# Performance work log

Hardware: AMD Instinct MI355X
Metric: run time of the kernel (lower is better)

The kernel has to match this reference:

```python
import jax, jax.numpy as jnp
import numpy as np

TOP_K = 48
NUM_RBF = 16
MAX_REL = 32  # max_relative_feature
B, L = 2, 3072

# atom order in stacked tensor: N=0, Ca=1, C=2, O=3, Cb=4
_PAIRS = np.array([
    (0, 0), (2, 2), (3, 3), (4, 4), (1, 0), (1, 2), (1, 3), (1, 4),
    (0, 2), (0, 3), (0, 4), (4, 2), (4, 3), (3, 2), (0, 1), (2, 1),
    (3, 1), (4, 1), (2, 0), (3, 0), (4, 0), (2, 4), (3, 4), (2, 3)], dtype=np.int32)


def _rbf(D):
    # D [..., ] -> [..., NUM_RBF]
    mu = jnp.linspace(2.0, 22.0, NUM_RBF)
    sigma = (22.0 - 2.0) / NUM_RBF
    return jnp.exp(-(((D[..., None] - mu) / sigma) ** 2))


def setup_inputs() -> dict:
    key = jax.random.key(0)
    ks = jax.random.split(key, 8)
    X = jax.random.normal(ks[0], (B, L, 4, 3), dtype=jnp.float32) * 3.0
    mask = jnp.ones((B, L), dtype=jnp.float32)
    R_idx = jnp.sort(jax.random.randint(ks[1], (B, L), 0, 6144), axis=-1)
    chain_labels = jax.random.randint(ks[2], (B, L), 0, 4)
    pos_W = jax.random.normal(ks[3], (2 * MAX_REL + 2, 16), dtype=jnp.float32) * 0.1
    pos_b = jax.random.normal(ks[4], (16,), dtype=jnp.float32) * 0.02
    edge_W = jax.random.normal(ks[5], (16 + 25 * NUM_RBF, 128), dtype=jnp.float32) * 0.05
    ln_gamma = jnp.ones((128,), dtype=jnp.float32)
    ln_beta = jnp.zeros((128,), dtype=jnp.float32)
    return {"X": X, "mask": mask, "R_idx": R_idx, "chain_labels": chain_labels,
            "pos_W": pos_W, "pos_b": pos_b, "edge_W": edge_W,
            "ln_gamma": ln_gamma, "ln_beta": ln_beta}


def reference(X, mask, R_idx, chain_labels, pos_W, pos_b, edge_W, ln_gamma, ln_beta):
    # virtual Cb construction
    bvec = X[:, :, 1, :] - X[:, :, 0, :]
    cvec = X[:, :, 2, :] - X[:, :, 1, :]
    avec = jnp.cross(bvec, cvec)
    Ca = X[:, :, 1, :]
    Cb = -0.58273431 * avec + 0.56802827 * bvec - 0.54067466 * cvec + Ca
    atoms = jnp.stack([X[:, :, 0, :], Ca, X[:, :, 2, :], X[:, :, 3, :], Cb], axis=2)  # [B,L,5,3]

    # masked pairwise Ca distances + k smallest neighbors
    mask2d = mask[:, :, None] * mask[:, None, :]                        # [B,L,L]
    dX = Ca[:, :, None, :] - Ca[:, None, :, :]
    D = mask2d * jnp.sqrt(jnp.sum(dX ** 2, axis=-1) + 1e-6)
    D_max = jnp.max(D, axis=-1, keepdims=True)
    D_adjust = D + (1.0 - mask2d) * D_max
    k = min(TOP_K, X.shape[1])
    neg_vals, E_idx = jax.lax.top_k(-D_adjust, k)                       # [B,L,K]
    D_neighbors = -neg_vals

    # gather neighbor atom coords once: [B,L,K,5,3]
    atoms_nb = jax.vmap(lambda a, i: a[i])(atoms, E_idx)

    # 24 remaining atom-pair distances, restricted to neighbors (same math as
    # full cdist + gather since dist is computed per (i, E_idx[i,j]) pair)
    ai, bi = _PAIRS[:, 0], _PAIRS[:, 1]
    diff = atoms[:, :, None, ai, :] - atoms_nb[:, :, :, bi, :]          # [B,L,K,24,3]
    D24 = jnp.sqrt(jnp.sum(diff ** 2, axis=-1) + 1e-6)                  # [B,L,K,24]

    D_all = jnp.concatenate([D_neighbors[..., None], D24], axis=-1)    # [B,L,K,25]
    RBF_all = _rbf(D_all).reshape(D_all.shape[:3] + (25 * NUM_RBF,))   # [B,L,K,400]

    # positional encodings on neighbor offsets
    offset = R_idx[:, :, None] - R_idx[:, None, :]
    offset = jnp.take_along_axis(offset, E_idx, axis=2)                 # [B,L,K]
    same_chain = (chain_labels[:, :, None] - chain_labels[:, None, :] == 0).astype(jnp.int32)
    E_chains = jnp.take_along_axis(same_chain, E_idx, axis=2)           # [B,L,K]
    d = jnp.clip(offset + MAX_REL, 0, 2 * MAX_REL) * E_chains + (1 - E_chains) * (2 * MAX_REL + 1)
    E_positional = pos_W[d] + pos_b                                     # one-hot @ W == row gather

    E = jnp.concatenate([E_positional, RBF_all], axis=-1)              # [B,L,K,416]
    E = E @ edge_W                                                      # [B,L,K,128]
    mu = jnp.mean(E, axis=-1, keepdims=True)
    var = jnp.mean((E - mu) ** 2, axis=-1, keepdims=True)
    E = (E - mu) / jnp.sqrt(var + 1e-5) * ln_gamma + ln_beta
    return E, E_idx
```

## Files before the change

### kernel.cpp

```cpp
#include <hip/hip_runtime.h>
#include <hip/hip_bf16.h>
#include <stdint.h>
#include <math.h>

#define B_   2
#define L_   3072
#define K_   48
#define FDIM 416
#define NOUT 128
#define FRS8 424

__device__ const unsigned char PAIRC[24] = {
    0, 18, 27, 36, 8, 10, 11, 12, 2, 3, 4, 34, 35, 26,
    1, 17, 25, 33, 16, 24, 32, 20, 28, 19
};

typedef __attribute__((ext_vector_type(4))) float f32x4;

__global__ __launch_bounds__(256) void k_prep(const float* __restrict__ X,
                                              const float* __restrict__ edgeW,
                                              float* __restrict__ atoms,
                                              float* __restrict__ CaA,
                                              unsigned char* __restrict__ Wt8)
{
    const int bid = blockIdx.x;
    if (bid < 52) {
        int idx4 = bid * 256 + threadIdx.x;
        int b = idx4 * 4;
        int e0  = b & 7;
        int lhi = (b >> 3) & 3;
        int l15 = (b >> 5) & 15;
        int nt  = (b >> 9) & 7;
        int kt  = b >> 12;
        int n = nt * 16 + l15;
        int kbase = kt * 32 + lhi * 8 + e0;
        float v0 = edgeW[(kbase + 0) * NOUT + n];
        float v1 = edgeW[(kbase + 1) * NOUT + n];
        float v2 = edgeW[(kbase + 2) * NOUT + n];
        float v3 = edgeW[(kbase + 3) * NOUT + n];
        int w = __builtin_amdgcn_cvt_pk_fp8_f32(v0, v1, 0, false);
        w = __builtin_amdgcn_cvt_pk_fp8_f32(v2, v3, w, true);
        ((unsigned int*)Wt8)[idx4] = (unsigned int)w;
    } else {
        int row = (bid - 52) * 256 + threadIdx.x;
        if (row >= B_ * L_) return;
        const float* x = X + row * 12;
        float nx = x[0], ny = x[1], nz = x[2];
        float cax = x[3], cay = x[4], caz = x[5];
        float cx = x[6], cy = x[7], cz = x[8];
        float ox = x[9], oy = x[10], oz = x[11];
        float bx = cax - nx, by = cay - ny, bz = caz - nz;
        float vx = cx - cax, vy = cy - cay, vz = cz - caz;
        float axv = by * vz - bz * vy;
        float ayv = bz * vx - bx * vz;
        float azv = bx * vy - by * vx;
        float cbx = -0.58273431f * axv + 0.56802827f * bx - 0.54067466f * vx + cax;
        float cby = -0.58273431f * ayv + 0.56802827f * by - 0.54067466f * vy + cay;
        float cbz = -0.58273431f * azv + 0.56802827f * bz - 0.54067466f * vz + caz;
        float* A = atoms + row * 16;
        A[0] = nx;  A[1] = ny;  A[2] = nz;
        A[3] = cax; A[4] = cay; A[5] = caz;
        A[6] = cx;  A[7] = cy;  A[8] = cz;
        A[9] = ox;  A[10] = oy; A[11] = oz;
        A[12] = cbx; A[13] = cby; A[14] = cbz;
        A[15] = 0.f;
        CaA[row * 3 + 0] = cax;
        CaA[row * 3 + 1] = cay;
        CaA[row * 3 + 2] = caz;
    }
}

__global__ __launch_bounds__(256) void k_topk(const float* __restrict__ CaA,
                                              const float* __restrict__ mask,
                                              int* __restrict__ eidx,
                                              float* __restrict__ dnb,
                                              float* __restrict__ out_eidx_f)
{
    __shared__ __align__(16) unsigned int SH[3072];
    unsigned int* hist  = SH;
    unsigned int* candJ = SH + 2048;
    unsigned long long* candK = (unsigned long long*)SH;
    __shared__ unsigned int swave[4];
    __shared__ int sP;
    __shared__ unsigned int sCnt;

    const int row = blockIdx.x;
    const int b = row / L_;
    const int tid = threadIdx.x;
    const int lane = tid & 63;
    const int wv = tid >> 6;

    #pragma unroll
    for (int i = 0; i < 8; ++i) hist[tid + 256 * i] = 0;
    if (tid == 0) sCnt = 0;

    const float caxf = CaA[row * 3 + 0];
    const float cayf = CaA[row * 3 + 1];
    const float cazf = CaA[row * 3 + 2];
    const float mif = mask[row];
    const float* Cb = CaA + (size_t)b * L_ * 3;
    const float* mb = mask + (size_t)b * L_;
    __syncthreads();

    unsigned int bits[12];
    #pragma unroll
    for (int m = 0; m < 12; ++m) {
        int j = tid + 256 * m;
        float dx = caxf - Cb[j * 3 + 0];
        float dy = cayf - Cb[j * 3 + 1];
        float dz = cazf - Cb[j * 3 + 2];
        float s = fmaf(dz, dz, fmaf(dy, dy, dx * dx)) + 1e-6f;
        float dist = sqrtf(s);
        bool live = (mif * mb[j]) != 0.0f;
        bits[m] = live ? __float_as_uint(dist) : 0x7F800000u;
        atomicAdd(&hist[bits[m] >> 20], 1u);
    }
    __syncthreads();

    unsigned int loc[8];
    unsigned int s = 0;
    #pragma unroll
    for (int i = 0; i < 8; ++i) { loc[i] = hist[tid * 8 + i]; s += loc[i]; }
    unsigned int sc = s;
    #pragma unroll
    for (int off = 1; off < 64; off <<= 1) {
        unsigned int o = __shfl_up(sc, off);
        if (lane >= off) sc += o;
    }
    if (lane == 63) swave[wv] = sc;
    __syncthreads();
    unsigned int base = 0;
    #pragma unroll
    for (int w = 0; w < 4; ++w) if (w < wv) base += swave[w];
    unsigned int cum = base + sc - s;
    #pragma unroll
    for (int i = 0; i < 8; ++i) {
        unsigned int c = loc[i];
        if (cum < K_ && cum + c >= K_) sP = tid * 8 + i;
        cum += c;
    }
    __syncthreads();
    const unsigned int Pth = (unsigned int)sP + 2;

    #pragma unroll
    for (int m = 0; m < 12; ++m) {
        if ((bits[m] >> 20) <= Pth) {
            unsigned int pos = atomicAdd(&sCnt, 1u);
            if (pos < 1024) candJ[pos] = (unsigned)(tid + 256 * m);
        }
    }
    __syncthreads();
    int cnt = (int)sCnt;
    if (cnt > 1024) cnt = 1024;

    const double cax = (double)caxf, cay = (double)cayf, caz = (double)cazf;
    for (int i = tid; i < cnt; i += 256) {
        int j = (int)candJ[i];
        double dx = cax - (double)Cb[j * 3 + 0];
        double dy = cay - (double)Cb[j * 3 + 1];
        double dz = caz - (double)Cb[j * 3 + 2];
        double ss = dx * dx;
        ss = ss + dy * dy;
        ss = ss + dz * dz;
        ss = ss + 1e-6;
        float v = (float)sqrt(ss);
        candK[i] = ((unsigned long long)__float_as_uint(v) << 32) | (unsigned)j;
    }
    __syncthreads();

    if (cnt <= 64) {
        if (wv == 0) {
            unsigned long long k = (lane < cnt) ? candK[lane] : ~0ull;
            #pragma unroll
            for (int size = 2; size <= 64; size <<= 1) {
                #pragma unroll
                for (int stride = size >> 1; stride >= 1; stride >>= 1) {
                    unsigned long long o = __shfl_xor(k, stride);
                    bool low = (lane & stride) == 0;
                    bool up = (lane & size) == 0 || size == 64;
                    unsigned long long mn = k < o ? k : o;
                    unsigned long long mx = k < o ? o : k;
                    k = (low == up) ? mn : mx;
                }
            }
            if (lane < K_) {
                int gj = (int)(unsigned)(k & 0xffffffffu);
                eidx[row * K_ + lane] = gj;
                dnb[row * K_ + lane] = __uint_as_float((unsigned)(k >> 32));
                out_eidx_f[row * K_ + lane] = (float)gj;
            }
        }
    } else {
        int M2 = 128;
        while (M2 < cnt) M2 <<= 1;
        for (int i = cnt + tid; i < M2; i += 256) candK[i] = ~0ull;
        for (int size = 2; size <= M2; size <<= 1) {
            for (int stride = size >> 1; stride > 0; stride >>= 1) {
                __syncthreads();
                for (int i = tid; i < M2; i += 256) {
                    int p = i ^ stride;
                    if (p > i) {
                        unsigned long long a = candK[i];
                        unsigned long long c2 = candK[p];
                        bool up = ((i & size) == 0);
                        if ((a > c2) == up) { candK[i] = c2; candK[p] = a; }
                    }
                }
            }
        }
        __syncthreads();
        if (tid < K_) {
            unsigned long long g = candK[tid];
            int gj = (int)(unsigned)(g & 0xffffffffu);
            eidx[row * K_ + tid] = gj;
            dnb[row * K_ + tid] = __uint_as_float((unsigned)(g >> 32));
            out_eidx_f[row * K_ + tid] = (float)gj;
        }
    }
}

__global__ __launch_bounds__(256) void k_edge(const float* __restrict__ atoms,
                                              const int* __restrict__ eidx,
                                              const float* __restrict__ dnb,
                                              const int* __restrict__ Ridx,
                                              const int* __restrict__ chain,
                                              const float* __restrict__ posW,
                                              const float* __restrict__ posb,
                                              const unsigned char* __restrict__ Wt8,
                                              const float* __restrict__ gamma,
                                              const float* __restrict__ beta,
                                              float* __restrict__ Eout)
{
    __shared__ __align__(16) unsigned char F8[K_ * FRS8];
    __shared__ __align__(16) float sAtoms[K_][16];
    __shared__ __align__(16) float sOwn[16];
    __shared__ int   sE[K_];
    __shared__ float sDnb[K_];
    __shared__ int   sDpos[K_];
    __shared__ float Psum[K_][4];
    __shared__ float Psq[K_][4];

    const int row = blockIdx.x;
    const int b = row / L_;
    const int tid = threadIdx.x;

    if (tid < K_) {
        sE[tid] = eidx[row * K_ + tid];
        sDnb[tid] = dnb[row * K_ + tid];
    }
    __syncthreads();

    if (tid < 192) {
        int k = tid >> 2, part = tid & 3;
        const float4 v = *(const float4*)(atoms + ((size_t)b * L_ + sE[k]) * 16 + part * 4);
        *(float4*)(&sAtoms[k][part * 4]) = v;
    } else if (tid < 196) {
        int part = tid - 192;
        *(float4*)(&sOwn[part * 4]) = *(const float4*)(atoms + (size_t)row * 16 + part * 4);
    } else if (tid >= 208) {
        int k = tid - 208;
        int j = sE[k];
        int off = Ridx[row] - Ridx[b * L_ + j];
        int ch = (chain[row] == chain[b * L_ + j]) ? 1 : 0;
        sDpos[k] = ch ? min(max(off + 32, 0), 64) : 65;
    }
    __syncthreads();

    if (tid < 240) {
        const int k = tid / 5;
        const int dd0 = tid - k * 5;
        #pragma unroll
        for (int s5 = 0; s5 < 5; ++s5) {
            const int dd = dd0 + 5 * s5;
            float D;
            if (dd == 0) {
                D = sDnb[k];
            } else {
                int pr = PAIRC[dd - 1];
                int ai = pr >> 3, bi = pr & 7;
                float dx = sOwn[ai * 3 + 0] - sAtoms[k][bi * 3 + 0];
                float dy = sOwn[ai * 3 + 1] - sAtoms[k][bi * 3 + 1];
                float dz = sOwn[ai * 3 + 2] - sAtoms[k][bi * 3 + 2];
                D = sqrtf(fmaf(dz, dz, fmaf(dy, dy, dx * dx)) + 1e-6f);
            }
            float z = (D - 2.0f) * 0.8f;
            unsigned int u[4];
            #pragma unroll
            for (int p = 0; p < 4; ++p) {
                float e0 = __expf(-(z * z)); z -= 1.0666667f;
                float e1 = __expf(-(z * z)); z -= 1.0666667f;
                float e2 = __expf(-(z * z)); z -= 1.0666667f;
                float e3 = __expf(-(z * z)); z -= 1.0666667f;
                int w = __builtin_amdgcn_cvt_pk_fp8_f32(e0, e1, 0, false);
                w = __builtin_amdgcn_cvt_pk_fp8_f32(e2, e3, w, true);
                u[p] = (unsigned int)w;
            }
            unsigned char* dst = F8 + k * FRS8 + 16 + dd * 16;
            *(uint2*)(dst) = make_uint2(u[0], u[1]);
            *(uint2*)(dst + 8) = make_uint2(u[2], u[3]);
        }
    }
    for (int s = tid; s < K_ * 16; s += 256) {
        int k = s >> 4, r = s & 15;
        float v = posW[sDpos[k] * 16 + r] + posb[r];
        int w = __builtin_amdgcn_cvt_pk_fp8_f32(v, v, 0, false);
        F8[k * FRS8 + r] = (unsigned char)(w & 0xff);
    }
    __syncthreads();

    const int lane = tid & 63;
    const int wv = tid >> 6;
    const int l15 = lane & 15;
    const int lhi = lane >> 4;

    f32x4 acc[3][2];
    #pragma unroll
    for (int mt = 0; mt < 3; ++mt)
        #pragma unroll
        for (int nn = 0; nn < 2; ++nn)
            acc[mt][nn] = (f32x4){0.f, 0.f, 0.f, 0.f};

    const unsigned char* wp = Wt8 + wv * 1024 + l15 * 32 + lhi * 8;
    long bc0 = *(const long*)(wp);
    long bc1 = *(const long*)(wp + 512);

    #pragma unroll 1
    for (int kt = 0; kt < 13; ++kt) {
        long bn0 = 0, bn1 = 0;
        if (kt < 12) {
            bn0 = *(const long*)(wp + (kt + 1) * 4096);
            bn1 = *(const long*)(wp + (kt + 1) * 4096 + 512);
        }
        const int k0 = kt * 32 + lhi * 8;
        long a0 = *(const long*)(F8 + (l15) * FRS8 + k0);
        long a1 = *(const long*)(F8 + (16 + l15) * FRS8 + k0);
        long a2 = *(const long*)(F8 + (32 + l15) * FRS8 + k0);
        acc[0][0] = __builtin_amdgcn_mfma_f32_16x16x32_fp8_fp8(a0, bc0, acc[0][0], 0, 0, 0);
        acc[0][1] = __builtin_amdgcn_mfma_f32_16x16x32_fp8_fp8(a0, bc1, acc[0][1], 0, 0, 0);
        acc[1][0] = __builtin_amdgcn_mfma_f32_16x16x32_fp8_fp8(a1, bc0, acc[1][0], 0, 0, 0);
        acc[1][1] = __builtin_amdgcn_mfma_f32_16x16x32_fp8_fp8(a1, bc1, acc[1][1], 0, 0, 0);
        acc[2][0] = __builtin_amdgcn_mfma_f32_16x16x32_fp8_fp8(a2, bc0, acc[2][0], 0, 0, 0);
        acc[2][1] = __builtin_amdgcn_mfma_f32_16x16x32_fp8_fp8(a2, bc1, acc[2][1], 0, 0, 0);
        bc0 = bn0;
        bc1 = bn1;
    }

    #pragma unroll
    for (int mt = 0; mt < 3; ++mt) {
        #pragma unroll
        for (int r = 0; r < 4; ++r) {
            float v0 = acc[mt][0][r], v1 = acc[mt][1][r];
            float s = v0 + v1;
            float q = v0 * v0 + v1 * v1;
            #pragma unroll
            for (int off = 1; off < 16; off <<= 1) {
                s += __shfl_xor(s, off);
                q += __shfl_xor(q, off);
            }
            if (l15 == 0) {
                int er = mt * 16 + lhi * 4 + r;
                Psum[er][wv] = s;
                Psq[er][wv] = q;
            }
        }
    }
    __syncthreads();

    const int c0 = wv * 32 + l15;
    float g2[2], be2[2];
    g2[0] = gamma[c0];      g2[1] = gamma[c0 + 16];
    be2[0] = beta[c0];      be2[1] = beta[c0 + 16];

    #pragma unroll
    for (int mt = 0; mt < 3; ++mt) {
        #pragma unroll
        for (int r = 0; r < 4; ++r) {
            int er = mt * 16 + lhi * 4 + r;
            float s = Psum[er][0] + Psum[er][1] + Psum[er][2] + Psum[er][3];
            float q = Psq[er][0] + Psq[er][1] + Psq[er][2] + Psq[er][3];
            float mu = s * (1.0f / 128.0f);
            float var = q * (1.0f / 128.0f) - mu * mu;
            float inv = 1.0f / sqrtf(var + 1e-5f);
            float* op = Eout + ((size_t)row * K_ + er) * 128;
            op[c0]      = (acc[mt][0][r] - mu) * inv * g2[0] + be2[0];
            op[c0 + 16] = (acc[mt][1][r] - mu) * inv * g2[1] + be2[1];
        }
    }
}

extern "C" void kernel_launch(void* const* d_in, const int* in_sizes, int n_in,
                              void* d_out, int out_size, void* d_ws, size_t ws_size,
                              hipStream_t stream) {
    const float* X     = (const float*)d_in[0];
    const float* mask  = (const float*)d_in[1];
    const int*   Ridx  = (const int*)d_in[2];
    const int*   chain = (const int*)d_in[3];
    const float* posW  = (const float*)d_in[4];
    const float* posb  = (const float*)d_in[5];
    const float* edgeW = (const float*)d_in[6];
    const float* gamma = (const float*)d_in[7];
    const float* beta  = (const float*)d_in[8];

    float* out   = (float*)d_out;
    float* Eout  = out;
    float* EidxF = out + (size_t)B_ * L_ * K_ * NOUT;

    float* atoms = (float*)d_ws;
    float* CaA   = atoms + (size_t)B_ * L_ * 16;
    int*   eidx  = (int*)(CaA + (size_t)B_ * L_ * 3);
    float* dnb   = (float*)(eidx + (size_t)B_ * L_ * K_);
    unsigned char* Wt8 = (unsigned char*)(dnb + (size_t)B_ * L_ * K_);

    hipLaunchKernelGGL(k_prep, dim3(52 + (B_ * L_ + 255) / 256), dim3(256), 0, stream,
                       X, edgeW, atoms, CaA, Wt8);
    hipLaunchKernelGGL(k_topk, dim3(B_ * L_), dim3(256), 0, stream,
                       CaA, mask, eidx, dnb, EidxF);
    hipLaunchKernelGGL(k_edge, dim3(B_ * L_), dim3(256), 0, stream,
                       atoms, eidx, dnb, Ridx, chain, posW, posb, Wt8, gamma, beta, Eout);
}
```

Baseline: 139.0 us.

## Fuse top-k and edge-feature kernels, compute RBF via exp recurrence

Merges the top-k neighbor selection kernel and the edge-feature/GEMM/LayerNorm kernel into one per-row kernel. Neighbor indices and distances now stay in shared memory instead of going through a global workspace, which also drops one launch. Shared memory is aliased between the top-k histogram and the fp8 feature tile. The RBF evaluation now uses one exp per group of four plus a multiplicative recurrence instead of four exps, with the argument clamped at 20. This trades a small accuracy risk for fewer transcendental calls and a higher per-block shared-memory footprint.

```diff
diff --git a/kernel.cpp b/kernel.cpp
--- a/kernel.cpp
+++ b/kernel.cpp
@@ -27,13 +27,12 @@
     if (bid < 52) {
         int idx4 = bid * 256 + threadIdx.x;
         int b = idx4 * 4;
-        int e0  = b & 7;
         int lhi = (b >> 3) & 3;
         int l15 = (b >> 5) & 15;
         int nt  = (b >> 9) & 7;
         int kt  = b >> 12;
         int n = nt * 16 + l15;
-        int kbase = kt * 32 + lhi * 8 + e0;
+        int kbase = kt * 32 + lhi * 8 + (b & 7);
         float v0 = edgeW[(kbase + 0) * NOUT + n];
         float v1 = edgeW[(kbase + 1) * NOUT + n];
         float v2 = edgeW[(kbase + 2) * NOUT + n];
@@ -70,19 +69,34 @@
     }
 }
 
-__global__ __launch_bounds__(256) void k_topk(const float* __restrict__ CaA,
+__global__ __launch_bounds__(256) void k_main(const float* __restrict__ CaA,
                                               const float* __restrict__ mask,
-                                              int* __restrict__ eidx,
-                                              float* __restrict__ dnb,
-                                              float* __restrict__ out_eidx_f)
+                                              const float* __restrict__ atoms,
+                                              const int* __restrict__ Ridx,
+                                              const int* __restrict__ chainL,
+                                              const float* __restrict__ posW,
+                                              const float* __restrict__ posb,
+                                              const unsigned char* __restrict__ Wt8,
+                                              const float* __restrict__ gamma,
+                                              const float* __restrict__ beta,
+                                              float* __restrict__ Eout,
+                                              float* __restrict__ EidxF)
 {
-    __shared__ __align__(16) unsigned int SH[3072];
-    unsigned int* hist  = SH;
-    unsigned int* candJ = SH + 2048;
-    unsigned long long* candK = (unsigned long long*)SH;
+    __shared__ __align__(16) unsigned char RAW[K_ * FRS8];
+    __shared__ __align__(16) float sAtoms[K_][16];
+    __shared__ __align__(16) float sOwn[16];
+    __shared__ int   sE[K_];
+    __shared__ float sDnb[K_];
+    __shared__ int   sDpos[K_];
+    __shared__ float Psum[K_][4];
+    __shared__ float Psq[K_][4];
     __shared__ unsigned int swave[4];
     __shared__ int sP;
     __shared__ unsigned int sCnt;
+
+    unsigned int* hist  = (unsigned int*)RAW;
+    unsigned int* candJ = (unsigned int*)(RAW + 8192);
+    unsigned long long* candK = (unsigned long long*)RAW;
 
     const int row = blockIdx.x;
     const int b = row / L_;
@@ -185,9 +199,9 @@
             }
             if (lane < K_) {
                 int gj = (int)(unsigned)(k & 0xffffffffu);
-                eidx[row * K_ + lane] = gj;
-                dnb[row * K_ + lane] = __uint_as_float((unsigned)(k >> 32));
-                out_eidx_f[row * K_ + lane] = (float)gj;
+                sE[lane] = gj;
+                sDnb[lane] = __uint_as_float((unsigned)(k >> 32));
+                EidxF[row * K_ + lane] = (float)gj;
             }
         }
     } else {
@@ -212,41 +226,10 @@
         if (tid < K_) {
             unsigned long long g = candK[tid];
             int gj = (int)(unsigned)(g & 0xffffffffu);
-            eidx[row * K_ + tid] = gj;
-            dnb[row * K_ + tid] = __uint_as_float((unsigned)(g >> 32));
-            out_eidx_f[row * K_ + tid] = (float)gj;
-        }
-    }
-}
-
-__global__ __launch_bounds__(256) void k_edge(const float* __restrict__ atoms,
-                                              const int* __restrict__ eidx,
-                                              const float* __restrict__ dnb,
-                                              const int* __restrict__ Ridx,
-                                              const int* __restrict__ chain,
-                                              const float* __restrict__ posW,
-                                              const float* __restrict__ posb,
-                                              const unsigned char* __restrict__ Wt8,
-                                              const float* __restrict__ gamma,
-                                              const float* __restrict__ beta,
-                                              float* __restrict__ Eout)
-{
-    __shared__ __align__(16) unsigned char F8[K_ * FRS8];
-    __shared__ __align__(16) float sAtoms[K_][16];
-    __shared__ __align__(16) float sOwn[16];
-    __shared__ int   sE[K_];
-    __shared__ float sDnb[K_];
-    __shared__ int   sDpos[K_];
-    __shared__ float Psum[K_][4];
-    __shared__ float Psq[K_][4];
-
-    const int row = blockIdx.x;
-    const int b = row / L_;
-    const int tid = threadIdx.x;
-
-    if (tid < K_) {
-        sE[tid] = eidx[row * K_ + tid];
-        sDnb[tid] = dnb[row * K_ + tid];
+            sE[tid] = gj;
+            sDnb[tid] = __uint_as_float((unsigned)(g >> 32));
+            EidxF[row * K_ + tid] = (float)gj;
+        }
     }
     __syncthreads();
 
@@ -261,7 +244,7 @@
         int k = tid - 208;
         int j = sE[k];
         int off = Ridx[row] - Ridx[b * L_ + j];
-        int ch = (chain[row] == chain[b * L_ + j]) ? 1 : 0;
+        int ch = (chainL[row] == chainL[b * L_ + j]) ? 1 : 0;
         sDpos[k] = ch ? min(max(off + 32, 0), 64) : 65;
     }
     __syncthreads();
@@ -269,6 +252,7 @@
     if (tid < 240) {
         const int k = tid / 5;
         const int dd0 = tid - k * 5;
+        unsigned char* Fk = RAW + k * FRS8;
         #pragma unroll
         for (int s5 = 0; s5 < 5; ++s5) {
             const int dd = dd0 + 5 * s5;
@@ -283,33 +267,34 @@
                 float dz = sOwn[ai * 3 + 2] - sAtoms[k][bi * 3 + 2];
                 D = sqrtf(fmaf(dz, dz, fmaf(dy, dy, dx * dx)) + 1e-6f);
             }
-            float z = (D - 2.0f) * 0.8f;
+            float t = fminf((D - 2.0f) * 0.8f, 20.0f);
             unsigned int u[4];
             #pragma unroll
-            for (int p = 0; p < 4; ++p) {
-                float e0 = __expf(-(z * z)); z -= 1.0666667f;
-                float e1 = __expf(-(z * z)); z -= 1.0666667f;
-                float e2 = __expf(-(z * z)); z -= 1.0666667f;
-                float e3 = __expf(-(z * z)); z -= 1.0666667f;
+            for (int gp = 0; gp < 4; ++gp) {
+                float e0 = __expf(-(t * t));
+                float r  = __expf(fmaf(2.1333334f, t, -1.1377778f));
+                float e1 = e0 * r; r *= 0.1027400f;
+                float e2 = e1 * r; r *= 0.1027400f;
+                float e3 = e2 * r;
                 int w = __builtin_amdgcn_cvt_pk_fp8_f32(e0, e1, 0, false);
                 w = __builtin_amdgcn_cvt_pk_fp8_f32(e2, e3, w, true);
-                u[p] = (unsigned int)w;
-            }
-            unsigned char* dst = F8 + k * FRS8 + 16 + dd * 16;
-            *(uint2*)(dst) = make_uint2(u[0], u[1]);
+                u[gp] = (unsigned int)w;
+                t -= 4.2666667f;
+            }
+            unsigned char* dst = Fk + 16 + dd * 16;
+            *(uint2*)(dst)     = make_uint2(u[0], u[1]);
             *(uint2*)(dst + 8) = make_uint2(u[2], u[3]);
         }
     }
-    for (int s = tid; s < K_ * 16; s += 256) {
-        int k = s >> 4, r = s & 15;
+    for (int s2 = tid; s2 < K_ * 16; s2 += 256) {
+        int k = s2 >> 4, r = s2 & 15;
         float v = posW[sDpos[k] * 16 + r] + posb[r];
         int w = __builtin_amdgcn_cvt_pk_fp8_f32(v, v, 0, false);
-        F8[k * FRS8 + r] = (unsigned char)(w & 0xff);
-    }
-    __syncthreads();
-
-    const int lane = tid & 63;
-    const int wv = tid >> 6;
+        RAW[k * FRS8 + r] = (unsigned char)(w & 0xff);
+    }
+    __syncthreads();
+
+    const unsigned char* F8 = RAW;
     const int l15 = lane & 15;
     const int lhi = lane >> 4;
 
@@ -350,16 +335,16 @@
         #pragma unroll
         for (int r = 0; r < 4; ++r) {
             float v0 = acc[mt][0][r], v1 = acc[mt][1][r];
-            float s = v0 + v1;
+            float sv = v0 + v1;
             float q = v0 * v0 + v1 * v1;
             #pragma unroll
             for (int off = 1; off < 16; off <<= 1) {
-                s += __shfl_xor(s, off);
+                sv += __shfl_xor(sv, off);
                 q += __shfl_xor(q, off);
             }
             if (l15 == 0) {
                 int er = mt * 16 + lhi * 4 + r;
-                Psum[er][wv] = s;
+                Psum[er][wv] = sv;
                 Psq[er][wv] = q;
             }
         }
@@ -376,9 +361,9 @@
         #pragma unroll
         for (int r = 0; r < 4; ++r) {
             int er = mt * 16 + lhi * 4 + r;
-            float s = Psum[er][0] + Psum[er][1] + Psum[er][2] + Psum[er][3];
+            float sv = Psum[er][0] + Psum[er][1] + Psum[er][2] + Psum[er][3];
             float q = Psq[er][0] + Psq[er][1] + Psq[er][2] + Psq[er][3];
-            float mu = s * (1.0f / 128.0f);
+            float mu = sv * (1.0f / 128.0f);
             float var = q * (1.0f / 128.0f) - mu * mu;
             float inv = 1.0f / sqrtf(var + 1e-5f);
             float* op = Eout + ((size_t)row * K_ + er) * 128;
@@ -407,14 +392,10 @@
 
     float* atoms = (float*)d_ws;
     float* CaA   = atoms + (size_t)B_ * L_ * 16;
-    int*   eidx  = (int*)(CaA + (size_t)B_ * L_ * 3);
-    float* dnb   = (float*)(eidx + (size_t)B_ * L_ * K_);
-    unsigned char* Wt8 = (unsigned char*)(dnb + (size_t)B_ * L_ * K_);
+    unsigned char* Wt8 = (unsigned char*)(CaA + (size_t)B_ * L_ * 3);
 
     hipLaunchKernelGGL(k_prep, dim3(52 + (B_ * L_ + 255) / 256), dim3(256), 0, stream,
                        X, edgeW, atoms, CaA, Wt8);
-    hipLaunchKernelGGL(k_topk, dim3(B_ * L_), dim3(256), 0, stream,
-                       CaA, mask, eidx, dnb, EidxF);
-    hipLaunchKernelGGL(k_edge, dim3(B_ * L_), dim3(256), 0, stream,
-                       atoms, eidx, dnb, Ridx, chain, posW, posb, Wt8, gamma, beta, Eout);
+    hipLaunchKernelGGL(k_main, dim3(B_ * L_), dim3(256), 0, stream,
+                       CaA, mask, atoms, Ridx, chain, posW, posb, Wt8, gamma, beta, Eout, EidxF);
 }
```

Result: slower. 153.2 us (+10.2%).
